# Performance work log

Hardware: AMD Instinct MI355X
Metric: run time of the kernel (lower is better)

Reference implementation:

```python
import jax, jax.numpy as jnp
import numpy as np

EPS = 1e-08

def qmul(a, b):
    # Hamilton product on trailing dim 4 (w, x, y, z)
    aw, av = a[..., :1], a[..., 1:]
    bw, bv = b[..., :1], b[..., 1:]
    w = aw * bw - jnp.sum(av * bv, axis=-1, keepdims=True)
    v = aw * bv + bw * av + jnp.cross(av, bv)
    return jnp.concatenate([w, v], axis=-1)

def qconj(q):
    return q * jnp.array([1.0, -1.0, -1.0, -1.0], dtype=q.dtype)

def qnormalize(q):
    return q / (jnp.linalg.norm(q, axis=-1, keepdims=True) + EPS)

def exp_map(v):
    # su(2) 3-vector -> unit quaternion
    theta = jnp.linalg.norm(v, axis=-1, keepdims=True) + EPS
    axis = v / theta
    return jnp.concatenate([jnp.cos(theta), axis * jnp.sin(theta)], axis=-1)

def setup_inputs() -> dict:
    key = jax.random.key(0)
    ks = jax.random.split(key, 6)
    B, D = 2048, 4096
    Q = D // 4  # 1024 quaternions
    x = jax.random.normal(ks[0], (B, D), dtype=jnp.float32)
    state = qnormalize(jax.random.normal(ks[1], (B, Q, 4), dtype=jnp.float32))
    W_phi = jax.random.normal(ks[2], (D, D), dtype=jnp.float32) / np.sqrt(D)
    b_phi = jnp.zeros((D,), dtype=jnp.float32)
    W_dde = jax.random.normal(ks[3], (Q, D), dtype=jnp.float32) / np.sqrt(D)
    b_dde = jnp.zeros((Q,), dtype=jnp.float32)
    return {"x": x, "state": state, "W_phi": W_phi, "b_phi": b_phi,
            "W_dde": W_dde, "b_dde": b_dde}

def reference(x, state, W_phi, b_phi, W_dde, b_dde):
    B = x.shape[0]
    Q = state.shape[1]
    # phi_gate: Linear(D, D), viewed as [B, Q, 4]
    v = (jnp.einsum('bd,ed->be', x, W_phi) + b_phi).reshape(B, Q, 4)
    rotation = exp_map(v[..., 1:])
    # reversible update: S_{t+1} = normalize(S_t (x) R_t)
    next_state = qnormalize(qmul(state, rotation))
    # diagnostics (no-grad in original)
    drift = jax.lax.stop_gradient(
        jnp.mean(jnp.abs(jnp.linalg.norm(next_state, axis=-1) - 1.0)))
    eta = drift  # SpectralShiftTracker eta
    # dde gate: Linear(D, Q) + sigmoid on flattened next_state
    gate = jax.nn.sigmoid(
        jnp.einsum('bd,qd->bq', next_state.reshape(B, -1), W_dde) + b_dde)
    final_state = state + gate[..., None] * (next_state - state)
    return (final_state, eta)
```

## Files before the change

### kernel.cpp

```cpp
#include <hip/hip_runtime.h>
#include <stdint.h>

#define GLOBAL_AS __attribute__((address_space(1)))
#define LDS_AS    __attribute__((address_space(3)))

typedef __attribute__((ext_vector_type(8))) short bf16x8;
typedef __attribute__((ext_vector_type(4))) float f32x4;

#define B_DIM 2048
#define D_DIM 4096
#define Q_DIM 1024
#define EPSF  1e-8f

__device__ __forceinline__ unsigned short f2bf(float f) {
  union { float f; unsigned int u; } v; v.f = f;
  unsigned int u = v.u;
  u += 0x7FFFu + ((u >> 16) & 1u);
  return (unsigned short)(u >> 16);
}

#define NX4    2097152u
#define NWPHI4 4194304u
#define NWDDE4 1048576u

__global__ __launch_bounds__(256) void k_convert(
    const float* __restrict__ x, const float* __restrict__ wphi,
    const float* __restrict__ wdde,
    unsigned short* __restrict__ xb, unsigned short* __restrict__ wphib,
    unsigned short* __restrict__ wddeb, float* __restrict__ drift) {
  unsigned int idx = blockIdx.x * 256u + threadIdx.x;
  if (idx == 0) *drift = 0.0f;
  const float4* s; ushort4* d; unsigned int local;
  if (idx < NX4)              { s = (const float4*)x;    d = (ushort4*)xb;    local = idx; }
  else if (idx < NX4 + NWPHI4){ s = (const float4*)wphi; d = (ushort4*)wphib; local = idx - NX4; }
  else                        { s = (const float4*)wdde; d = (ushort4*)wddeb; local = idx - (NX4 + NWPHI4); }
  float4 v = s[local];
  d[local] = make_ushort4(f2bf(v.x), f2bf(v.y), f2bf(v.z), f2bf(v.w));
}

__global__ __launch_bounds__(256) void k_gemm1(
    const unsigned short* __restrict__ A, const unsigned short* __restrict__ Bm,
    const float* __restrict__ bphi, const float* __restrict__ state,
    float* __restrict__ nsf ,
    unsigned short* __restrict__ nsb ,
    float* __restrict__ drift) {
  __shared__ __align__(16) unsigned short sAB[2 * 128 * 32];
  const int t = threadIdx.x;
  const int lane = t & 63;
  const int w = t >> 6;
  const int bn = blockIdx.x;
  const int bm = blockIdx.y;
  const int rowA0 = bm * 128;
  const int rowB0 = bn * 128;

  const int c0 = t, c1 = t + 256;
  const unsigned short* gA0 = A  + (size_t)(rowA0 + (c0 >> 2)) * D_DIM + (c0 & 3) * 8;
  const unsigned short* gA1 = A  + (size_t)(rowA0 + (c1 >> 2)) * D_DIM + (c1 & 3) * 8;
  const unsigned short* gB0 = Bm + (size_t)(rowB0 + (c0 >> 2)) * D_DIM + (c0 & 3) * 8;
  const unsigned short* gB1 = Bm + (size_t)(rowB0 + (c1 >> 2)) * D_DIM + (c1 & 3) * 8;
  unsigned short* lA0 = &sAB[c0 * 8];
  unsigned short* lA1 = &sAB[c1 * 8];
  unsigned short* lB0 = &sAB[4096 + c0 * 8];
  unsigned short* lB1 = &sAB[4096 + c1 * 8];

  f32x4 acc[4][4] = {};
  const int lm = lane & 15;
  const int lq = lane >> 4;
  const int mbase = (w >> 1) * 64;
  const int nbase = (w & 1) * 64;

  for (int k0 = 0; k0 < D_DIM; k0 += 32) {
    __builtin_amdgcn_global_load_lds((const GLOBAL_AS unsigned int*)(gA0 + k0), (LDS_AS unsigned int*)lA0, 16, 0, 0);
    __builtin_amdgcn_global_load_lds((const GLOBAL_AS unsigned int*)(gA1 + k0), (LDS_AS unsigned int*)lA1, 16, 0, 0);
    __builtin_amdgcn_global_load_lds((const GLOBAL_AS unsigned int*)(gB0 + k0), (LDS_AS unsigned int*)lB0, 16, 0, 0);
    __builtin_amdgcn_global_load_lds((const GLOBAL_AS unsigned int*)(gB1 + k0), (LDS_AS unsigned int*)lB1, 16, 0, 0);
    __syncthreads();
    bf16x8 af[4], bfr[4];
#pragma unroll
    for (int i = 0; i < 4; ++i)
      af[i] = *(const bf16x8*)&sAB[(mbase + i * 16 + lm) * 32 + lq * 8];
#pragma unroll
    for (int j = 0; j < 4; ++j)
      bfr[j] = *(const bf16x8*)&sAB[4096 + (nbase + j * 16 + lm) * 32 + lq * 8];
#pragma unroll
    for (int i = 0; i < 4; ++i)
#pragma unroll
      for (int j = 0; j < 4; ++j)
        acc[i][j] = __builtin_amdgcn_mfma_f32_16x16x32_bf16(af[i], bfr[j], acc[i][j], 0, 0, 0);
    __syncthreads();
  }

  float* cscr = ((float*)sAB) + w * 1024;
  float driftLocal = 0.0f;
  const int colBase = rowB0 + nbase;
  const int qBase = colBase >> 2;
#pragma unroll
  for (int i = 0; i < 4; ++i) {
    __syncthreads();
#pragma unroll
    for (int j = 0; j < 4; ++j)
#pragma unroll
      for (int r = 0; r < 4; ++r)
        cscr[(lq * 4 + r) * 64 + j * 16 + lm] = acc[i][j][r];
    __syncthreads();
#pragma unroll
    for (int s = 0; s < 4; ++s) {
      const int qlin = s * 64 + lane;
      const int lrow = qlin >> 4;
      const int qc = qlin & 15;
      float4 vq = *(const float4*)&cscr[lrow * 64 + qc * 4];
      float4 bq = ((const float4*)bphi)[qBase + qc];
      float vx = vq.y + bq.y, vy = vq.z + bq.z, vz = vq.w + bq.w;
      float th = sqrtf(vx * vx + vy * vy + vz * vz) + EPSF;
      float st = sinf(th), ct = cosf(th);
      float sc = st / th;
      float rw = ct, rx = vx * sc, ry = vy * sc, rz = vz * sc;
      const int grow = rowA0 + mbase + i * 16 + lrow;
      const size_t qgi = (size_t)grow * Q_DIM + (qBase + qc);
      float4 sq = ((const float4*)state)[qgi];
      float aw = sq.x, ax = sq.y, ay = sq.z, az = sq.w;
      float nw = aw * rw - ax * rx - ay * ry - az * rz;
      float nx = aw * rx + rw * ax + (ay * rz - az * ry);
      float ny = aw * ry + rw * ay + (az * rx - ax * rz);
      float nz = aw * rz + rw * az + (ax * ry - ay * rx);
      float nrm = sqrtf(nw * nw + nx * nx + ny * ny + nz * nz);
      float invn = 1.0f / (nrm + EPSF);
      nw *= invn; nx *= invn; ny *= invn; nz *= invn;
      float n2 = sqrtf(nw * nw + nx * nx + ny * ny + nz * nz);
      driftLocal += fabsf(n2 - 1.0f);
      float4 o; o.x = nw; o.y = nx; o.z = ny; o.w = nz;
      ((float4*)nsf)[qgi] = o;
      ((ushort4*)nsb)[qgi] = make_ushort4(f2bf(nw), f2bf(nx), f2bf(ny), f2bf(nz));
    }
  }
#pragma unroll
  for (int off = 32; off > 0; off >>= 1) driftLocal += __shfl_down(driftLocal, off);
  if (lane == 0) atomicAdd(drift, driftLocal);
}

__global__ __launch_bounds__(256) void k_gemm2(
    const unsigned short* __restrict__ A ,
    const unsigned short* __restrict__ Bm ,
    const float* __restrict__ bdde, const float* __restrict__ state,
    float* __restrict__ out ) {
  __shared__ unsigned short sA[128 * 32];
  __shared__ unsigned short sB[64 * 32];
  const int t = threadIdx.x;
  const int lane = t & 63;
  const int w = t >> 6;
  const int bn = blockIdx.x;
  const int bm = blockIdx.y;
  const int rowA0 = bm * 128;
  const int rowB0 = bn * 64;
  const int c0 = t, c1 = t + 256;
  const unsigned short* gA0 = A  + (size_t)(rowA0 + (c0 >> 2)) * D_DIM + (c0 & 3) * 8;
  const unsigned short* gA1 = A  + (size_t)(rowA0 + (c1 >> 2)) * D_DIM + (c1 & 3) * 8;
  const unsigned short* gB0 = Bm + (size_t)(rowB0 + (c0 >> 2)) * D_DIM + (c0 & 3) * 8;
  unsigned short* lA0 = &sA[c0 * 8];
  unsigned short* lA1 = &sA[c1 * 8];
  unsigned short* lB0 = &sB[c0 * 8];

  f32x4 acc[4][2] = {};
  const int lm = lane & 15, lq = lane >> 4;
  const int mbase = (w >> 1) * 64, nbase = (w & 1) * 32;

  for (int k0 = 0; k0 < D_DIM; k0 += 32) {
    __builtin_amdgcn_global_load_lds((const GLOBAL_AS unsigned int*)(gA0 + k0), (LDS_AS unsigned int*)lA0, 16, 0, 0);
    __builtin_amdgcn_global_load_lds((const GLOBAL_AS unsigned int*)(gA1 + k0), (LDS_AS unsigned int*)lA1, 16, 0, 0);
    __builtin_amdgcn_global_load_lds((const GLOBAL_AS unsigned int*)(gB0 + k0), (LDS_AS unsigned int*)lB0, 16, 0, 0);
    __syncthreads();
    bf16x8 af[4], bfr[2];
#pragma unroll
    for (int i = 0; i < 4; ++i)
      af[i] = *(const bf16x8*)&sA[(mbase + i * 16 + lm) * 32 + lq * 8];
#pragma unroll
    for (int j = 0; j < 2; ++j)
      bfr[j] = *(const bf16x8*)&sB[(nbase + j * 16 + lm) * 32 + lq * 8];
#pragma unroll
    for (int i = 0; i < 4; ++i)
#pragma unroll
      for (int j = 0; j < 2; ++j)
        acc[i][j] = __builtin_amdgcn_mfma_f32_16x16x32_bf16(af[i], bfr[j], acc[i][j], 0, 0, 0);
    __syncthreads();
  }
#pragma unroll
  for (int i = 0; i < 4; ++i) {
    const int rb = rowA0 + mbase + i * 16 + lq * 4;
#pragma unroll
    for (int j = 0; j < 2; ++j) {
      const int q = rowB0 + nbase + j * 16 + lm;
      const float bias = bdde[q];
#pragma unroll
      for (int r = 0; r < 4; ++r) {
        const int row = rb + r;
        float z = acc[i][j][r] + bias;
        float gate = 1.0f / (1.0f + expf(-z));
        size_t qi = (size_t)row * Q_DIM + q;
        float4 sq = ((const float4*)state)[qi];
        float4 nq = ((const float4*)out)[qi];
        float4 f;
        f.x = sq.x + gate * (nq.x - sq.x);
        f.y = sq.y + gate * (nq.y - sq.y);
        f.z = sq.z + gate * (nq.z - sq.z);
        f.w = sq.w + gate * (nq.w - sq.w);
        ((float4*)out)[qi] = f;
      }
    }
  }
}

__global__ void k_eta(const float* __restrict__ drift, float* __restrict__ out_eta) {
  *out_eta = *drift * (1.0f / 2097152.0f);
}

extern "C" void kernel_launch(void* const* d_in, const int* in_sizes, int n_in,
                              void* d_out, int out_size, void* d_ws, size_t ws_size,
                              hipStream_t stream) {
  const float* x     = (const float*)d_in[0];
  const float* state = (const float*)d_in[1];
  const float* wphi  = (const float*)d_in[2];
  const float* bphi  = (const float*)d_in[3];
  const float* wdde  = (const float*)d_in[4];
  const float* bdde  = (const float*)d_in[5];
  float* out = (float*)d_out;
  char* ws = (char*)d_ws;
  unsigned short* xb    = (unsigned short*)(ws);
  unsigned short* wphib = (unsigned short*)(ws + 16777216);
  unsigned short* wddeb = (unsigned short*)(ws + 50331648);
  unsigned short* nsb   = (unsigned short*)(ws + 58720256);
  float* drift          = (float*)(ws + 75497472);

  k_convert<<<28672, 256, 0, stream>>>(x, wphi, wdde, xb, wphib, wddeb, drift);
  dim3 g1(32, 16);
  k_gemm1<<<g1, 256, 0, stream>>>(xb, wphib, bphi, state, out, nsb, drift);
  dim3 g2(16, 16);
  k_gemm2<<<g2, 256, 0, stream>>>(nsb, wddeb, bdde, state, out);
  k_eta<<<1, 1, 0, stream>>>(drift, out + (out_size - 1));
}
```

Baseline: 375.0 us.

## Double K-tile depth with XOR-swizzled LDS layout and smaller gemm2 tiles

Both GEMM kernels now stage a 64-wide K slice per iteration instead of 32, which halves the number of barrier pairs per K loop. The LDS layout XOR-swizzles the 16-byte column chunks by row so the wider-row fragment reads avoid bank conflicts. gemm2 also drops from 128x64 to 64x64 tiles with a doubled grid, giving more blocks on the device for the smaller second GEMM. The cost is more LDS per block (32 KB in gemm1) and less operand reuse per block in gemm2.

```diff
diff --git a/kernel.cpp b/kernel.cpp
--- a/kernel.cpp
+++ b/kernel.cpp
@@ -38,13 +38,14 @@
   d[local] = make_ushort4(f2bf(v.x), f2bf(v.y), f2bf(v.z), f2bf(v.w));
 }
 
+
 __global__ __launch_bounds__(256) void k_gemm1(
     const unsigned short* __restrict__ A, const unsigned short* __restrict__ Bm,
     const float* __restrict__ bphi, const float* __restrict__ state,
     float* __restrict__ nsf ,
     unsigned short* __restrict__ nsb ,
     float* __restrict__ drift) {
-  __shared__ __align__(16) unsigned short sAB[2 * 128 * 32];
+  __shared__ __align__(16) unsigned short sAB[2 * 128 * 64];
   const int t = threadIdx.x;
   const int lane = t & 63;
   const int w = t >> 6;
@@ -53,40 +54,50 @@
   const int rowA0 = bm * 128;
   const int rowB0 = bn * 128;
 
-  const int c0 = t, c1 = t + 256;
-  const unsigned short* gA0 = A  + (size_t)(rowA0 + (c0 >> 2)) * D_DIM + (c0 & 3) * 8;
-  const unsigned short* gA1 = A  + (size_t)(rowA0 + (c1 >> 2)) * D_DIM + (c1 & 3) * 8;
-  const unsigned short* gB0 = Bm + (size_t)(rowB0 + (c0 >> 2)) * D_DIM + (c0 & 3) * 8;
-  const unsigned short* gB1 = Bm + (size_t)(rowB0 + (c1 >> 2)) * D_DIM + (c1 & 3) * 8;
-  unsigned short* lA0 = &sAB[c0 * 8];
-  unsigned short* lA1 = &sAB[c1 * 8];
-  unsigned short* lB0 = &sAB[4096 + c0 * 8];
-  unsigned short* lB1 = &sAB[4096 + c1 * 8];
+  const unsigned short* gA[4]; const unsigned short* gB[4];
+  unsigned short *lA[4], *lB[4];
+#pragma unroll
+  for (int p = 0; p < 4; ++p) {
+    const int c = t + p * 256;
+    const int row = c >> 3;
+    const int kcg = (c & 7) ^ (row & 7);
+    gA[p] = A  + (size_t)(rowA0 + row) * D_DIM + kcg * 8;
+    gB[p] = Bm + (size_t)(rowB0 + row) * D_DIM + kcg * 8;
+    lA[p] = &sAB[c * 8];
+    lB[p] = &sAB[8192 + c * 8];
+  }
 
   f32x4 acc[4][4] = {};
   const int lm = lane & 15;
   const int lq = lane >> 4;
   const int mbase = (w >> 1) * 64;
   const int nbase = (w & 1) * 64;
-
-  for (int k0 = 0; k0 < D_DIM; k0 += 32) {
-    __builtin_amdgcn_global_load_lds((const GLOBAL_AS unsigned int*)(gA0 + k0), (LDS_AS unsigned int*)lA0, 16, 0, 0);
-    __builtin_amdgcn_global_load_lds((const GLOBAL_AS unsigned int*)(gA1 + k0), (LDS_AS unsigned int*)lA1, 16, 0, 0);
-    __builtin_amdgcn_global_load_lds((const GLOBAL_AS unsigned int*)(gB0 + k0), (LDS_AS unsigned int*)lB0, 16, 0, 0);
-    __builtin_amdgcn_global_load_lds((const GLOBAL_AS unsigned int*)(gB1 + k0), (LDS_AS unsigned int*)lB1, 16, 0, 0);
-    __syncthreads();
-    bf16x8 af[4], bfr[4];
-#pragma unroll
-    for (int i = 0; i < 4; ++i)
-      af[i] = *(const bf16x8*)&sAB[(mbase + i * 16 + lm) * 32 + lq * 8];
-#pragma unroll
-    for (int j = 0; j < 4; ++j)
-      bfr[j] = *(const bf16x8*)&sAB[4096 + (nbase + j * 16 + lm) * 32 + lq * 8];
-#pragma unroll
-    for (int i = 0; i < 4; ++i)
+  const int rsw = lm & 7;
+
+  for (int k0 = 0; k0 < D_DIM; k0 += 64) {
+#pragma unroll
+    for (int p = 0; p < 4; ++p) {
+      __builtin_amdgcn_global_load_lds((const GLOBAL_AS unsigned int*)(gA[p] + k0), (LDS_AS unsigned int*)lA[p], 16, 0, 0);
+      __builtin_amdgcn_global_load_lds((const GLOBAL_AS unsigned int*)(gB[p] + k0), (LDS_AS unsigned int*)lB[p], 16, 0, 0);
+    }
+    __syncthreads();
+#pragma unroll
+    for (int ks = 0; ks < 2; ++ks) {
+      const int kc = ks * 4 + lq;
+      const int csw = (kc ^ rsw) * 8;
+      bf16x8 af[4], bfr[4];
+#pragma unroll
+      for (int i = 0; i < 4; ++i)
+        af[i] = *(const bf16x8*)&sAB[(mbase + i * 16 + lm) * 64 + csw];
 #pragma unroll
       for (int j = 0; j < 4; ++j)
-        acc[i][j] = __builtin_amdgcn_mfma_f32_16x16x32_bf16(af[i], bfr[j], acc[i][j], 0, 0, 0);
+        bfr[j] = *(const bf16x8*)&sAB[8192 + (nbase + j * 16 + lm) * 64 + csw];
+#pragma unroll
+      for (int i = 0; i < 4; ++i)
+#pragma unroll
+        for (int j = 0; j < 4; ++j)
+          acc[i][j] = __builtin_amdgcn_mfma_f32_16x16x32_bf16(af[i], bfr[j], acc[i][j], 0, 0, 0);
+    }
     __syncthreads();
   }
 
@@ -143,48 +154,61 @@
     const unsigned short* __restrict__ Bm ,
     const float* __restrict__ bdde, const float* __restrict__ state,
     float* __restrict__ out ) {
-  __shared__ unsigned short sA[128 * 32];
-  __shared__ unsigned short sB[64 * 32];
+  __shared__ __align__(16) unsigned short sAB[2 * 64 * 64];
   const int t = threadIdx.x;
   const int lane = t & 63;
   const int w = t >> 6;
   const int bn = blockIdx.x;
   const int bm = blockIdx.y;
-  const int rowA0 = bm * 128;
+  const int rowA0 = bm * 64;
   const int rowB0 = bn * 64;
-  const int c0 = t, c1 = t + 256;
-  const unsigned short* gA0 = A  + (size_t)(rowA0 + (c0 >> 2)) * D_DIM + (c0 & 3) * 8;
-  const unsigned short* gA1 = A  + (size_t)(rowA0 + (c1 >> 2)) * D_DIM + (c1 & 3) * 8;
-  const unsigned short* gB0 = Bm + (size_t)(rowB0 + (c0 >> 2)) * D_DIM + (c0 & 3) * 8;
-  unsigned short* lA0 = &sA[c0 * 8];
-  unsigned short* lA1 = &sA[c1 * 8];
-  unsigned short* lB0 = &sB[c0 * 8];
-
-  f32x4 acc[4][2] = {};
+
+  const unsigned short* gA[2]; const unsigned short* gB[2];
+  unsigned short *lA[2], *lB[2];
+#pragma unroll
+  for (int p = 0; p < 2; ++p) {
+    const int c = t + p * 256;
+    const int row = c >> 3;
+    const int kcg = (c & 7) ^ (row & 7);
+    gA[p] = A  + (size_t)(rowA0 + row) * D_DIM + kcg * 8;
+    gB[p] = Bm + (size_t)(rowB0 + row) * D_DIM + kcg * 8;
+    lA[p] = &sAB[c * 8];
+    lB[p] = &sAB[4096 + c * 8];
+  }
+
+  f32x4 acc[2][2] = {};
   const int lm = lane & 15, lq = lane >> 4;
-  const int mbase = (w >> 1) * 64, nbase = (w & 1) * 32;
-
-  for (int k0 = 0; k0 < D_DIM; k0 += 32) {
-    __builtin_amdgcn_global_load_lds((const GLOBAL_AS unsigned int*)(gA0 + k0), (LDS_AS unsigned int*)lA0, 16, 0, 0);
-    __builtin_amdgcn_global_load_lds((const GLOBAL_AS unsigned int*)(gA1 + k0), (LDS_AS unsigned int*)lA1, 16, 0, 0);
-    __builtin_amdgcn_global_load_lds((const GLOBAL_AS unsigned int*)(gB0 + k0), (LDS_AS unsigned int*)lB0, 16, 0, 0);
-    __syncthreads();
-    bf16x8 af[4], bfr[2];
-#pragma unroll
-    for (int i = 0; i < 4; ++i)
-      af[i] = *(const bf16x8*)&sA[(mbase + i * 16 + lm) * 32 + lq * 8];
-#pragma unroll
-    for (int j = 0; j < 2; ++j)
-      bfr[j] = *(const bf16x8*)&sB[(nbase + j * 16 + lm) * 32 + lq * 8];
-#pragma unroll
-    for (int i = 0; i < 4; ++i)
+  const int mbase = (w >> 1) * 32, nbase = (w & 1) * 32;
+  const int rsw = lm & 7;
+
+  for (int k0 = 0; k0 < D_DIM; k0 += 64) {
+#pragma unroll
+    for (int p = 0; p < 2; ++p) {
+      __builtin_amdgcn_global_load_lds((const GLOBAL_AS unsigned int*)(gA[p] + k0), (LDS_AS unsigned int*)lA[p], 16, 0, 0);
+      __builtin_amdgcn_global_load_lds((const GLOBAL_AS unsigned int*)(gB[p] + k0), (LDS_AS unsigned int*)lB[p], 16, 0, 0);
+    }
+    __syncthreads();
+#pragma unroll
+    for (int ks = 0; ks < 2; ++ks) {
+      const int kc = ks * 4 + lq;
+      const int csw = (kc ^ rsw) * 8;
+      bf16x8 af[2], bfr[2];
+#pragma unroll
+      for (int i = 0; i < 2; ++i)
+        af[i] = *(const bf16x8*)&sAB[(mbase + i * 16 + lm) * 64 + csw];
 #pragma unroll
       for (int j = 0; j < 2; ++j)
-        acc[i][j] = __builtin_amdgcn_mfma_f32_16x16x32_bf16(af[i], bfr[j], acc[i][j], 0, 0, 0);
-    __syncthreads();
-  }
-#pragma unroll
-  for (int i = 0; i < 4; ++i) {
+        bfr[j] = *(const bf16x8*)&sAB[4096 + (nbase + j * 16 + lm) * 64 + csw];
+#pragma unroll
+      for (int i = 0; i < 2; ++i)
+#pragma unroll
+        for (int j = 0; j < 2; ++j)
+          acc[i][j] = __builtin_amdgcn_mfma_f32_16x16x32_bf16(af[i], bfr[j], acc[i][j], 0, 0, 0);
+    }
+    __syncthreads();
+  }
+#pragma unroll
+  for (int i = 0; i < 2; ++i) {
     const int rb = rowA0 + mbase + i * 16 + lq * 4;
 #pragma unroll
     for (int j = 0; j < 2; ++j) {
@@ -233,7 +257,7 @@
   k_convert<<<28672, 256, 0, stream>>>(x, wphi, wdde, xb, wphib, wddeb, drift);
   dim3 g1(32, 16);
   k_gemm1<<<g1, 256, 0, stream>>>(xb, wphib, bphi, state, out, nsb, drift);
-  dim3 g2(16, 16);
+  dim3 g2(16, 32);
   k_gemm2<<<g2, 256, 0, stream>>>(nsb, wddeb, bdde, state, out);
   k_eta<<<1, 1, 0, stream>>>(drift, out + (out_size - 1));
 }
```

Measured after the change: 331.0 us. 11.7% less time.
